# Kernel optimization log

Hardware: AMD Instinct MI355X
Metric: run time of the kernel (lower is better)

The kernel has to match this reference:

```python
import jax, jax.numpy as jnp
import numpy as np

D_MODEL = 1024
N_HEADS = 16
D_Q = D_MODEL // N_HEADS
NEG = float(-2**32 + 1)


def setup_inputs() -> dict:
    key = jax.random.key(0)
    ks = jax.random.split(key, 8)
    B, L = 8, 1024
    q = jax.random.normal(ks[0], (B, L, D_MODEL), dtype=jnp.float32)
    k = jax.random.normal(ks[1], (B, L, D_MODEL), dtype=jnp.float32)
    # causal subsequent mask: 1 above the diagonal (positions to be masked)
    subseq_mask = jnp.broadcast_to(
        jnp.triu(jnp.ones((L, L), dtype=jnp.int32), k=1), (B, L, L))
    s = 1.0 / np.sqrt(D_MODEL)
    Wq = jax.random.normal(ks[2], (D_MODEL, D_MODEL), dtype=jnp.float32) * s
    Wk = jax.random.normal(ks[3], (D_MODEL, D_MODEL), dtype=jnp.float32) * s
    Wv = jax.random.normal(ks[4], (D_MODEL, D_MODEL), dtype=jnp.float32) * s
    bq = jax.random.normal(ks[5], (D_MODEL,), dtype=jnp.float32) * 0.01
    bk = jax.random.normal(ks[6], (D_MODEL,), dtype=jnp.float32) * 0.01
    bv = jax.random.normal(ks[7], (D_MODEL,), dtype=jnp.float32) * 0.01
    return {"q": q, "k": k, "subseq_mask": subseq_mask,
            "Wq": Wq, "bq": bq, "Wk": Wk, "bk": bk, "Wv": Wv, "bv": bv}


def reference(q, k, subseq_mask, Wq, bq, Wk, bk, Wv, bv):
    B, Lq, _ = q.shape
    Lk = k.shape[1]
    residual = q
    # projections; heads laid out as (H, B, L, d_q) matching torch permute(2,0,1,3)
    qp = (q @ Wq + bq).reshape(B, Lq, N_HEADS, D_Q).transpose(2, 0, 1, 3)
    kp = (k @ Wk + bk).reshape(B, Lk, N_HEADS, D_Q).transpose(2, 0, 1, 3)
    vp = (k @ Wv + bv).reshape(B, Lk, N_HEADS, D_Q).transpose(2, 0, 1, 3)
    # scaled scores: (H, B, Lq, Lk)
    scores = jnp.einsum('hbqd,hbkd->hbqk', qp, kp) / np.sqrt(D_Q)
    # key mask from PROJECTED k (faithful to source)
    key_masks = jnp.sign(jnp.abs(jnp.sum(kp, -1)))          # (H, B, Lk)
    scores = jnp.where(key_masks[:, :, None, :] == 0, NEG, scores)
    # subsequence (causal) mask, replicated over heads
    scores = jnp.where(subseq_mask[None, :, :, :] == 1, NEG, scores)
    attn = jax.nn.softmax(scores, axis=-1)
    # post-softmax query mask from PROJECTED q (faithful to source)
    query_masks = jnp.sign(jnp.abs(jnp.sum(qp, -1)))        # (H, B, Lq)
    attn = attn * query_masks[:, :, :, None]
    # dropout is identity in eval/reference mode
    out = jnp.einsum('hbqk,hbkd->hbqd', attn, vp)           # (H, B, Lq, d_q)
    out = out.transpose(1, 2, 0, 3).reshape(B, Lq, N_HEADS * D_Q)
    return out + residual
```

## Files before the change

kernel.cpp:

```cpp
#include <hip/hip_runtime.h>
#include <cstdint>
#include <cstddef>

#define DM 1024
#define NH 16
#define DQ 64
#define NB 8
#define LSEQ 1024

typedef __attribute__((ext_vector_type(8))) short short8;
typedef __attribute__((ext_vector_type(4))) float floatx4;

__device__ __forceinline__ unsigned short f2bf(float f) {
  union { float f; unsigned u; } v; v.f = f;
  unsigned r = v.u + 0x7FFFu + ((v.u >> 16) & 1u);
  return (unsigned short)(r >> 16);
}
__device__ __forceinline__ float bf2f(unsigned short u) {
  union { unsigned u; float f; } v; v.u = ((unsigned)u) << 16;
  return v.f;
}

__device__ __forceinline__ void async_load16(const void* g, void* l) {
  __builtin_amdgcn_global_load_lds(
      (const __attribute__((address_space(1))) unsigned int*)g,
      (__attribute__((address_space(3))) unsigned int*)l, 16, 0, 0);
}

__global__ void convert_qk(const float* __restrict__ q, const float* __restrict__ k,
                           unsigned short* __restrict__ qb, unsigned short* __restrict__ kb) {
  size_t i = ((size_t)blockIdx.x * 256 + threadIdx.x) * 4;
  float4 a = *(const float4*)&q[i];
  ushort4 r;
  r.x = f2bf(a.x); r.y = f2bf(a.y); r.z = f2bf(a.z); r.w = f2bf(a.w);
  *(ushort4*)&qb[i] = r;
  float4 b = *(const float4*)&k[i];
  ushort4 s;
  s.x = f2bf(b.x); s.y = f2bf(b.y); s.z = f2bf(b.z); s.w = f2bf(b.w);
  *(ushort4*)&kb[i] = s;
}

__global__ void transpose_w(const float* __restrict__ Wq, const float* __restrict__ Wk,
                            const float* __restrict__ Wv, unsigned short* __restrict__ Wt) {
  int z = blockIdx.z;
  const float* W = (z == 0) ? Wq : (z == 1) ? Wk : Wv;
  __shared__ float tile[32][33];
  int n0 = blockIdx.x * 32, k0 = blockIdx.y * 32;
  int tx = threadIdx.x;
  for (int j = threadIdx.y; j < 32; j += 8)
    tile[j][tx] = W[(size_t)(k0 + j) * DM + n0 + tx];
  __syncthreads();
  unsigned short* o = Wt + (size_t)z * DM * DM;
  for (int j = threadIdx.y; j < 32; j += 8)
    o[(size_t)(n0 + j) * DM + k0 + tx] = f2bf(tile[tx][j]);
}

__global__ __launch_bounds__(256, 4) void gemm_proj(
    const unsigned short* __restrict__ qb, const unsigned short* __restrict__ kb,
    const unsigned short* __restrict__ Wt,
    const float* __restrict__ bq, const float* __restrict__ bk, const float* __restrict__ bv,
    const float* __restrict__ ,
    unsigned short* __restrict__ Pq, unsigned short* __restrict__ Pk,
    unsigned short* __restrict__ Pvt,
    float* __restrict__ qmask, float* __restrict__ kmask) {
  const int z = blockIdx.z;
  const unsigned short* A = (z == 0) ? qb : kb;
  const unsigned short* Bt = Wt + (size_t)z * DM * DM;
  const float* bias = (z == 0) ? bq : (z == 1) ? bk : bv;

  __shared__ unsigned short smem[16384];
  unsigned short* As = smem;
  unsigned short* Bs = smem + 8192;

  const int tid = threadIdx.x;
  const int lane = tid & 63;
  const int wave = tid >> 6;
  const int l16 = lane & 15, quad = lane >> 4;
  const int wm = wave & 1, wn = wave >> 1;
  const int rowBase = blockIdx.x * 128;
  const int colBase = blockIdx.y * 128;

  floatx4 acc[4][4];
  const floatx4 zf = {0.f, 0.f, 0.f, 0.f};
#pragma unroll
  for (int i = 0; i < 4; i++)
#pragma unroll
    for (int j = 0; j < 4; j++) acc[i][j] = zf;

  const int srl = lane >> 3;
  const int sl7 = lane & 7;

  for (int kt = 0; kt < DM; kt += 64) {
#pragma unroll
    for (int cc = wave; cc < 16; cc += 4) {
      const int rl = cc * 8 + srl;
      const int ck = (sl7 ^ (rl & 7)) * 8;
      async_load16(A + (size_t)(rowBase + rl) * DM + kt + ck, &As[cc * 512]);
      async_load16(Bt + (size_t)(colBase + rl) * DM + kt + ck, &Bs[cc * 512]);
    }
    __syncthreads();

#pragma unroll
    for (int c = 0; c < 2; c++) {
      const int chnk = ((c << 2) + quad) ^ (l16 & 7);
      short8 af[4], bfr[4];
#pragma unroll
      for (int i = 0; i < 4; i++)
        af[i] = *(const short8*)&As[(wm * 64 + i * 16 + l16) * 64 + chnk * 8];
#pragma unroll
      for (int j = 0; j < 4; j++)
        bfr[j] = *(const short8*)&Bs[(wn * 64 + j * 16 + l16) * 64 + chnk * 8];
#pragma unroll
      for (int i = 0; i < 4; i++)
#pragma unroll
        for (int j = 0; j < 4; j++)
          acc[i][j] = __builtin_amdgcn_mfma_f32_16x16x32_bf16(af[i], bfr[j], acc[i][j], 0, 0, 0);
    }
    __syncthreads();
  }

#pragma unroll
  for (int j = 0; j < 4; j++) {
    const float bj = bias[colBase + wn * 64 + j * 16 + l16];
#pragma unroll
    for (int i = 0; i < 4; i++)
#pragma unroll
      for (int r = 0; r < 4; r++) acc[i][j][r] += bj;
  }

  if (z < 2) {
    float* mask = (z == 0) ? qmask : kmask;
    const int h = (colBase >> 6) + wn;
#pragma unroll
    for (int i = 0; i < 4; i++)
#pragma unroll
      for (int r = 0; r < 4; r++) {
        float rs = acc[i][0][r] + acc[i][1][r] + acc[i][2][r] + acc[i][3][r];
        rs += __shfl_xor(rs, 1);
        rs += __shfl_xor(rs, 2);
        rs += __shfl_xor(rs, 4);
        rs += __shfl_xor(rs, 8);
        if (l16 == 0) {
          const int row = rowBase + wm * 64 + i * 16 + quad * 4 + r;
          mask[((size_t)((row >> 10) * NH + h)) * LSEQ + (row & 1023)] = (rs != 0.f) ? 1.f : 0.f;
        }
      }
    unsigned short* P = (z == 0) ? Pq : Pk;
#pragma unroll
    for (int j = 0; j < 4; j++) {
      const int col = colBase + wn * 64 + j * 16 + l16;
      const int hh = col >> 6, d = col & 63;
#pragma unroll
      for (int i = 0; i < 4; i++) {
        const int row0 = rowBase + wm * 64 + i * 16 + quad * 4;
#pragma unroll
        for (int r = 0; r < 4; r++) {
          const int rr = row0 + r;
          P[((size_t)((rr >> 10) * NH + hh) * LSEQ + (rr & 1023)) * DQ + d] = f2bf(acc[i][j][r]);
        }
      }
    }
  } else {
    const int b = rowBase >> 10;
    const int l0r = rowBase & 1023;
#pragma unroll
    for (int j = 0; j < 4; j++) {
      __syncthreads();
#pragma unroll
      for (int i = 0; i < 4; i++) {
        ushort4 v;
        v.x = f2bf(acc[i][j][0]); v.y = f2bf(acc[i][j][1]);
        v.z = f2bf(acc[i][j][2]); v.w = f2bf(acc[i][j][3]);
        *(ushort4*)&smem[(wn * 16 + l16) * 136 + wm * 64 + i * 16 + quad * 4] = v;
      }
      __syncthreads();
      const int c = tid >> 3, seg = tid & 7;
      const int col = colBase + (c >> 4) * 64 + j * 16 + (c & 15);
      const int hh = col >> 6, d = col & 63;
      int4 t0 = *(const int4*)&smem[c * 136 + seg * 16];
      int4 t1 = *(const int4*)&smem[c * 136 + seg * 16 + 8];
      const size_t g = ((size_t)((b * NH + hh) * DQ + d)) * LSEQ + l0r + seg * 16;
      *(int4*)&Pvt[g] = t0;
      *(int4*)&Pvt[g + 8] = t1;
    }
  }
}

__global__ __launch_bounds__(256, 4) void attn_kernel(
    const unsigned short* __restrict__ Q, const unsigned short* __restrict__ K,
    const unsigned short* __restrict__ Vt,
    const float* __restrict__ kmask, const float* __restrict__ qmask,
    const float* __restrict__ qin, float* __restrict__ out) {
  const int bh = blockIdx.x;
  const int qblk = 7 - blockIdx.y;
  const int b = bh >> 4, h = bh & 15;
  const size_t base = (size_t)bh * LSEQ * DQ;

  const int tid = threadIdx.x;
  const int lane = tid & 63;
  const int wave = tid >> 6;
  const int l16 = lane & 15, quad = lane >> 4;
  const int qw = qblk * 128 + wave * 32;

  __shared__ unsigned short Ks[2 * 4096];
  __shared__ unsigned short Vs[2 * 4096];
  __shared__ unsigned short Ps[4][2304];

  short8 qf[2][2];
#pragma unroll
  for (int sub = 0; sub < 2; sub++)
#pragma unroll
    for (int c = 0; c < 2; c++) {
      short8 t = *(const short8*)&Q[base + (size_t)(qw + sub * 16 + l16) * DQ + c * 32 + quad * 8];
#pragma unroll
      for (int e = 0; e < 8; e++) t[e] = (short)f2bf(bf2f((unsigned short)t[e]) * 0.125f);
      qf[sub][c] = t;
    }

  const floatx4 zf = {0.f, 0.f, 0.f, 0.f};
  floatx4 o[2][4];
#pragma unroll
  for (int sub = 0; sub < 2; sub++)
#pragma unroll
    for (int jj = 0; jj < 4; jj++) o[sub][jj] = zf;
  float l_p[2][4] = {{0.f, 0.f, 0.f, 0.f}, {0.f, 0.f, 0.f, 0.f}};

  const int swz = (quad ^ (l16 & 7)) * 8;
  const int swz2 = ((quad + 4) ^ (l16 & 7)) * 8;
  const int vswz = (quad ^ (l16 >> 1)) * 8;
  const int vswz2 = ((quad + 4) ^ (l16 >> 1)) * 8;

  const int srl = (lane >> 3);
  const int ktiles = (qblk + 1) * 2;
  const int tmax = 2 * qblk + (wave >> 1);

  {
#pragma unroll
    for (int cc = wave; cc < 8; cc += 4) {
      const int rl = cc * 8 + srl;
      const int ck = ((lane & 7) ^ (rl & 7)) * 8;
      async_load16(&K[base + (size_t)rl * DQ + ck], &Ks[cc * 512]);
      const int cv = ((lane & 7) ^ ((rl >> 1) & 7)) * 8;
      async_load16(&Vt[base + (size_t)rl * LSEQ + cv], &Vs[cc * 512]);
    }
  }
  __syncthreads();

  for (int t = 0; t < ktiles; t++) {
    const int cur = t & 1;
    const int kt = t * 64;
    const bool live = (t <= tmax);

    float km[4];
    if (live) {
#pragma unroll
      for (int ct = 0; ct < 4; ct++) km[ct] = kmask[(size_t)bh * LSEQ + kt + ct * 16 + l16];
    }

    if (t + 1 < ktiles) {
      const int nkt = kt + 64;
      const int nb = (cur ^ 1) * 4096;
#pragma unroll
      for (int cc = wave; cc < 8; cc += 4) {
        const int rl = cc * 8 + srl;
        const int ck = ((lane & 7) ^ (rl & 7)) * 8;
        async_load16(&K[base + (size_t)(nkt + rl) * DQ + ck], &Ks[nb + cc * 512]);
        const int cv = ((lane & 7) ^ ((rl >> 1) & 7)) * 8;
        async_load16(&Vt[base + (size_t)rl * LSEQ + nkt + cv], &Vs[nb + cc * 512]);
      }
    }

    if (live) {
      const unsigned short* Kb = &Ks[cur * 4096];
      const unsigned short* Vb = &Vs[cur * 4096];
      const bool diag = (t == tmax);

#pragma unroll
      for (int sub = 0; sub < 2; sub++) {
        floatx4 s[4];
#pragma unroll
        for (int ct = 0; ct < 4; ct++) {
          const int kr = (ct * 16 + l16) * 64;
          const short8 kf0 = *(const short8*)&Kb[kr + swz];
          const short8 kf1 = *(const short8*)&Kb[kr + swz2];
          floatx4 sv = zf;
          sv = __builtin_amdgcn_mfma_f32_16x16x32_bf16(qf[sub][0], kf0, sv, 0, 0, 0);
          sv = __builtin_amdgcn_mfma_f32_16x16x32_bf16(qf[sub][1], kf1, sv, 0, 0, 0);
          s[ct] = sv;
        }
        const int row0 = qw + sub * 16 + quad * 4;
        unsigned short* pw = &Ps[wave][(sub * 16 + quad * 4) * 72];
        if (diag) {
#pragma unroll
          for (int ct = 0; ct < 4; ct++) {
            const int col = kt + ct * 16 + l16;
#pragma unroll
            for (int r = 0; r < 4; r++) {
              float e = __expf(s[ct][r]) * km[ct];
              e = (col <= row0 + r) ? e : 0.f;
              l_p[sub][r] += e;
              pw[r * 72 + ct * 16 + l16] = f2bf(e);
            }
          }
        } else {
#pragma unroll
          for (int ct = 0; ct < 4; ct++) {
#pragma unroll
            for (int r = 0; r < 4; r++) {
              float e = __expf(s[ct][r]) * km[ct];
              l_p[sub][r] += e;
              pw[r * 72 + ct * 16 + l16] = f2bf(e);
            }
          }
        }
      }
      asm volatile("s_waitcnt lgkmcnt(0)" ::: "memory");

      short8 pf[2][2];
#pragma unroll
      for (int sub = 0; sub < 2; sub++) {
        pf[sub][0] = *(const short8*)&Ps[wave][(sub * 16 + l16) * 72 + quad * 8];
        pf[sub][1] = *(const short8*)&Ps[wave][(sub * 16 + l16) * 72 + 32 + quad * 8];
      }
#pragma unroll
      for (int jj = 0; jj < 4; jj++) {
        const int vr = (jj * 16 + l16) * 64;
        const short8 vf0 = *(const short8*)&Vb[vr + vswz];
        const short8 vf1 = *(const short8*)&Vb[vr + vswz2];
#pragma unroll
        for (int sub = 0; sub < 2; sub++) {
          o[sub][jj] = __builtin_amdgcn_mfma_f32_16x16x32_bf16(pf[sub][0], vf0, o[sub][jj], 0, 0, 0);
          o[sub][jj] = __builtin_amdgcn_mfma_f32_16x16x32_bf16(pf[sub][1], vf1, o[sub][jj], 0, 0, 0);
        }
      }
    }
    __syncthreads();
  }

  const int hd = h * DQ;
#pragma unroll
  for (int sub = 0; sub < 2; sub++)
#pragma unroll
    for (int r = 0; r < 4; r++) {
      float lv = l_p[sub][r];
      lv += __shfl_xor(lv, 1);
      lv += __shfl_xor(lv, 2);
      lv += __shfl_xor(lv, 4);
      lv += __shfl_xor(lv, 8);
      const int row = qw + sub * 16 + quad * 4 + r;
      const float inv = qmask[(size_t)bh * LSEQ + row] / lv;
#pragma unroll
      for (int jj = 0; jj < 4; jj++) {
        const size_t oi = ((size_t)(b * LSEQ + row)) * DM + hd + jj * 16 + l16;
        out[oi] = o[sub][jj][r] * inv + qin[oi];
      }
    }
}

extern "C" void kernel_launch(void* const* d_in, const int* in_sizes, int n_in,
                              void* d_out, int out_size, void* d_ws, size_t ws_size,
                              hipStream_t stream) {
  const float* q = (const float*)d_in[0];
  const float* k = (const float*)d_in[1];
  const float* Wq = (const float*)d_in[3];
  const float* bq = (const float*)d_in[4];
  const float* Wk = (const float*)d_in[5];
  const float* bk = (const float*)d_in[6];
  const float* Wv = (const float*)d_in[7];
  const float* bv = (const float*)d_in[8];
  float* out = (float*)d_out;

  char* w = (char*)d_ws;
  unsigned short* qb = (unsigned short*)(w + 0);
  unsigned short* kb = (unsigned short*)(w + 16777216);
  unsigned short* Wt = (unsigned short*)(w + 33554432);
  unsigned short* Pq = (unsigned short*)(w + 39845888);
  unsigned short* Pk = (unsigned short*)(w + 56623104);
  unsigned short* Pvt = (unsigned short*)(w + 73400320);
  float* qmask = (float*)(w + 90177536);
  float* kmask = (float*)(w + 90701824);

  convert_qk<<<8192, 256, 0, stream>>>(q, k, qb, kb);
  transpose_w<<<dim3(32, 32, 3), dim3(32, 8), 0, stream>>>(Wq, Wk, Wv, Wt);
  gemm_proj<<<dim3(64, 8, 3), 256, 0, stream>>>(qb, kb, Wt, bq, bk, bv, nullptr,
                                                Pq, Pk, Pvt, qmask, kmask);
  attn_kernel<<<dim3(128, 8), 256, 0, stream>>>(Pq, Pk, Pvt, kmask, qmask, q, out);
}
```

Baseline: 259.8 us.

## Rewrite projection GEMM as 256x256 tile, 8-wave double-buffered pipelined kernel

The projection GEMM moves from 128x128 tiles with 4 waves and a single LDS buffer to 256x256 tiles with 8 waves, 128KB of double-buffered LDS, and a four-phase schedule. That schedule interleaves async global-to-LDS staging of the next K-slices with MFMA phases, and raises wave priority around the MFMAs. The V-transpose epilogue now goes through per-wave LDS staging instead of block-wide barriers. The aim is to hide global load latency and improve reuse per tile. In exchange, the grid is much smaller (384 blocks), which may underfill the GPU, and register pressure rises.

```diff
diff --git a/kernel.cpp b/kernel.cpp
--- a/kernel.cpp
+++ b/kernel.cpp
@@ -55,133 +55,212 @@
     o[(size_t)(n0 + j) * DM + k0 + tx] = f2bf(tile[tx][j]);
 }
 
-__global__ __launch_bounds__(256, 4) void gemm_proj(
-    const unsigned short* __restrict__ qb, const unsigned short* __restrict__ kb,
+#define HT0 0
+#define HT1 8192
+#define HT2 16384
+#define HT3 24576
+
+#define STAGE(REGB, SRCP, ROW0, KTV)                                      \
+  {                                                                       \
+    const unsigned short* sp_ = (SRCP) + (size_t)(ROW0) * DM + (KTV);     \
+    async_load16(sp_, &smem[(REGB) + wave * 512]);                        \
+    async_load16(sp_ + 64 * DM, &smem[(REGB) + 4096 + wave * 512]);       \
+  }
+
+#define LOAD_A(QA)                                                        \
+  {                                                                       \
+    _Pragma("unroll")                                                     \
+    for (int i_ = 0; i_ < 4; ++i_) {                                      \
+      const int ar_ = abase + ((QA) * 64 + i_ * 16 + l16) * 64;           \
+      af[i_][0] = *(const short8*)&smem[ar_ + x0];                        \
+      af[i_][1] = *(const short8*)&smem[ar_ + x1];                        \
+    }                                                                     \
+  }
+
+#define LOAD_B(QB)                                                        \
+  {                                                                       \
+    _Pragma("unroll")                                                     \
+    for (int j_ = 0; j_ < 2; ++j_) {                                      \
+      const int br_ = bbase + ((QB) * 32 + j_ * 16 + l16) * 64;           \
+      bqf[QB][j_][0] = *(const short8*)&smem[br_ + x0];                   \
+      bqf[QB][j_][1] = *(const short8*)&smem[br_ + x1];                   \
+    }                                                                     \
+  }
+
+#define PHASE_MFMA(RI, CI)                                                        \
+  {                                                                               \
+    __builtin_amdgcn_s_setprio(1);                                                \
+    _Pragma("unroll")                                                             \
+    for (int i_ = 0; i_ < 4; ++i_) {                                              \
+      _Pragma("unroll")                                                           \
+      for (int j_ = 0; j_ < 2; ++j_) {                                            \
+        acc[(RI) + i_][(CI) + j_] = __builtin_amdgcn_mfma_f32_16x16x32_bf16(      \
+            af[i_][0], bqf[(CI) >> 1][j_][0], acc[(RI) + i_][(CI) + j_], 0, 0, 0);\
+        acc[(RI) + i_][(CI) + j_] = __builtin_amdgcn_mfma_f32_16x16x32_bf16(      \
+            af[i_][1], bqf[(CI) >> 1][j_][1], acc[(RI) + i_][(CI) + j_], 0, 0, 0);\
+      }                                                                           \
+    }                                                                             \
+    __builtin_amdgcn_s_setprio(0);                                                \
+  }
+
+__global__ __launch_bounds__(512, 2) void gemm_proj(
+    const unsigned short* __restrict__ qbp, const unsigned short* __restrict__ kbp,
     const unsigned short* __restrict__ Wt,
-    const float* __restrict__ bq, const float* __restrict__ bk, const float* __restrict__ bv,
-    const float* __restrict__ ,
+    const float* __restrict__ bqv, const float* __restrict__ bkv, const float* __restrict__ bvv,
     unsigned short* __restrict__ Pq, unsigned short* __restrict__ Pk,
     unsigned short* __restrict__ Pvt,
     float* __restrict__ qmask, float* __restrict__ kmask) {
   const int z = blockIdx.z;
-  const unsigned short* A = (z == 0) ? qb : kb;
-  const unsigned short* Bt = Wt + (size_t)z * DM * DM;
-  const float* bias = (z == 0) ? bq : (z == 1) ? bk : bv;
-
-  __shared__ unsigned short smem[16384];
-  unsigned short* As = smem;
-  unsigned short* Bs = smem + 8192;
+  const unsigned short* Asrc = (z == 0) ? qbp : kbp;
+  const unsigned short* Bsrc = Wt + (size_t)z * DM * DM;
+  const float* bias = (z == 0) ? bqv : (z == 1) ? bkv : bvv;
+
+  __shared__ unsigned short smem[65536];
 
   const int tid = threadIdx.x;
   const int lane = tid & 63;
   const int wave = tid >> 6;
   const int l16 = lane & 15, quad = lane >> 4;
-  const int wm = wave & 1, wn = wave >> 1;
-  const int rowBase = blockIdx.x * 128;
-  const int colBase = blockIdx.y * 128;
-
-  floatx4 acc[4][4];
+  const int wm = wave >> 2, wn = wave & 3;
+  const int rowBase = blockIdx.x * 256;
+  const int colBase = blockIdx.y * 256;
+
+  const int srow = wave * 8 + (lane >> 3);
+  const int scol = ((lane & 7) ^ (lane >> 3)) * 8;
+  const unsigned short* Ap = Asrc + (size_t)srow * DM + scol;
+  const unsigned short* Bp = Bsrc + (size_t)srow * DM + scol;
+  const int x0 = (quad ^ (l16 & 7)) * 8;
+  const int x1 = ((quad + 4) ^ (l16 & 7)) * 8;
+
+  floatx4 acc[8][4];
   const floatx4 zf = {0.f, 0.f, 0.f, 0.f};
 #pragma unroll
-  for (int i = 0; i < 4; i++)
+  for (int i = 0; i < 8; i++)
 #pragma unroll
     for (int j = 0; j < 4; j++) acc[i][j] = zf;
 
-  const int srl = lane >> 3;
-  const int sl7 = lane & 7;
-
-  for (int kt = 0; kt < DM; kt += 64) {
-#pragma unroll
-    for (int cc = wave; cc < 16; cc += 4) {
-      const int rl = cc * 8 + srl;
-      const int ck = (sl7 ^ (rl & 7)) * 8;
-      async_load16(A + (size_t)(rowBase + rl) * DM + kt + ck, &As[cc * 512]);
-      async_load16(Bt + (size_t)(colBase + rl) * DM + kt + ck, &Bs[cc * 512]);
-    }
-    __syncthreads();
-
-#pragma unroll
-    for (int c = 0; c < 2; c++) {
-      const int chnk = ((c << 2) + quad) ^ (l16 & 7);
-      short8 af[4], bfr[4];
-#pragma unroll
-      for (int i = 0; i < 4; i++)
-        af[i] = *(const short8*)&As[(wm * 64 + i * 16 + l16) * 64 + chnk * 8];
-#pragma unroll
-      for (int j = 0; j < 4; j++)
-        bfr[j] = *(const short8*)&Bs[(wn * 64 + j * 16 + l16) * 64 + chnk * 8];
-#pragma unroll
-      for (int i = 0; i < 4; i++)
-#pragma unroll
-        for (int j = 0; j < 4; j++)
-          acc[i][j] = __builtin_amdgcn_mfma_f32_16x16x32_bf16(af[i], bfr[j], acc[i][j], 0, 0, 0);
-    }
-    __syncthreads();
-  }
-
-#pragma unroll
-  for (int j = 0; j < 4; j++) {
-    const float bj = bias[colBase + wn * 64 + j * 16 + l16];
-#pragma unroll
-    for (int i = 0; i < 4; i++)
-#pragma unroll
-      for (int r = 0; r < 4; r++) acc[i][j][r] += bj;
+  short8 af[4][2];
+  short8 bqf[2][2][2];
+
+  STAGE(HT0, Ap, rowBase, 0);
+  STAGE(HT1, Ap, rowBase + 128, 0);
+  STAGE(HT2, Bp, colBase, 0);
+  STAGE(HT3, Bp, colBase + 128, 0);
+  STAGE(32768 + HT2, Bp, colBase, 64);
+  STAGE(32768 + HT3, Bp, colBase + 128, 64);
+  asm volatile("s_waitcnt vmcnt(4)" ::: "memory");
+  __builtin_amdgcn_s_barrier();
+
+  for (int t = 0; t < 16; ++t) {
+    const int bufb = (t & 1) << 15;
+    const int bufn = bufb ^ 32768;
+    const int abase = bufb + wm * 8192;
+    const int bbase = bufb + HT2 + (wn >> 1) * 8192 + (wn & 1) * 4096;
+    const int kt1 = (t + 1) * 64;
+    const int kt2 = (t + 2) * 64;
+
+    LOAD_A(0);
+    LOAD_B(0);
+    if (t < 15) STAGE(bufn + HT0, Ap, rowBase, kt1);
+    __builtin_amdgcn_s_barrier();
+    asm volatile("s_waitcnt lgkmcnt(0)" ::: "memory");
+    PHASE_MFMA(0, 0);
+    __builtin_amdgcn_s_barrier();
+
+    LOAD_B(1);
+    if (t < 15) STAGE(bufn + HT1, Ap, rowBase + 128, kt1);
+    __builtin_amdgcn_s_barrier();
+    asm volatile("s_waitcnt lgkmcnt(0)" ::: "memory");
+    PHASE_MFMA(0, 2);
+    __builtin_amdgcn_s_barrier();
+
+    LOAD_A(1);
+    if (t < 14) STAGE(bufb + HT2, Bp, colBase, kt2);
+    __builtin_amdgcn_s_barrier();
+    asm volatile("s_waitcnt lgkmcnt(0)" ::: "memory");
+    PHASE_MFMA(4, 2);
+    __builtin_amdgcn_s_barrier();
+
+    if (t < 14) {
+      STAGE(bufb + HT3, Bp, colBase + 128, kt2);
+      asm volatile("s_waitcnt vmcnt(4)" ::: "memory");
+    } else {
+      asm volatile("s_waitcnt vmcnt(0)" ::: "memory");
+    }
+    __builtin_amdgcn_s_barrier();
+    PHASE_MFMA(4, 0);
+    __builtin_amdgcn_s_barrier();
+  }
+
+#pragma unroll
+  for (int ci = 0; ci < 4; ++ci) {
+    const float bj = bias[colBase + wn * 64 + ci * 16 + l16];
+#pragma unroll
+    for (int ri = 0; ri < 8; ++ri)
+#pragma unroll
+      for (int r = 0; r < 4; ++r) acc[ri][ci][r] += bj;
   }
 
   if (z < 2) {
     float* mask = (z == 0) ? qmask : kmask;
     const int h = (colBase >> 6) + wn;
 #pragma unroll
-    for (int i = 0; i < 4; i++)
-#pragma unroll
-      for (int r = 0; r < 4; r++) {
-        float rs = acc[i][0][r] + acc[i][1][r] + acc[i][2][r] + acc[i][3][r];
+    for (int ri = 0; ri < 8; ++ri)
+#pragma unroll
+      for (int r = 0; r < 4; ++r) {
+        float rs = acc[ri][0][r] + acc[ri][1][r] + acc[ri][2][r] + acc[ri][3][r];
         rs += __shfl_xor(rs, 1);
         rs += __shfl_xor(rs, 2);
         rs += __shfl_xor(rs, 4);
         rs += __shfl_xor(rs, 8);
         if (l16 == 0) {
-          const int row = rowBase + wm * 64 + i * 16 + quad * 4 + r;
+          const int row = rowBase + wm * 128 + ri * 16 + quad * 4 + r;
           mask[((size_t)((row >> 10) * NH + h)) * LSEQ + (row & 1023)] = (rs != 0.f) ? 1.f : 0.f;
         }
       }
     unsigned short* P = (z == 0) ? Pq : Pk;
 #pragma unroll
-    for (int j = 0; j < 4; j++) {
-      const int col = colBase + wn * 64 + j * 16 + l16;
+    for (int ci = 0; ci < 4; ++ci) {
+      const int col = colBase + wn * 64 + ci * 16 + l16;
       const int hh = col >> 6, d = col & 63;
 #pragma unroll
-      for (int i = 0; i < 4; i++) {
-        const int row0 = rowBase + wm * 64 + i * 16 + quad * 4;
-#pragma unroll
-        for (int r = 0; r < 4; r++) {
+      for (int ri = 0; ri < 8; ++ri) {
+        const int row0 = rowBase + wm * 128 + ri * 16 + quad * 4;
+#pragma unroll
+        for (int r = 0; r < 4; ++r) {
           const int rr = row0 + r;
-          P[((size_t)((rr >> 10) * NH + hh) * LSEQ + (rr & 1023)) * DQ + d] = f2bf(acc[i][j][r]);
+          P[((size_t)((rr >> 10) * NH + hh) * LSEQ + (rr & 1023)) * DQ + d] = f2bf(acc[ri][ci][r]);
         }
       }
     }
   } else {
     const int b = rowBase >> 10;
     const int l0r = rowBase & 1023;
-#pragma unroll
-    for (int j = 0; j < 4; j++) {
-      __syncthreads();
-#pragma unroll
-      for (int i = 0; i < 4; i++) {
-        ushort4 v;
-        v.x = f2bf(acc[i][j][0]); v.y = f2bf(acc[i][j][1]);
-        v.z = f2bf(acc[i][j][2]); v.w = f2bf(acc[i][j][3]);
-        *(ushort4*)&smem[(wn * 16 + l16) * 136 + wm * 64 + i * 16 + quad * 4] = v;
-      }
-      __syncthreads();
-      const int c = tid >> 3, seg = tid & 7;
-      const int col = colBase + (c >> 4) * 64 + j * 16 + (c & 15);
-      const int hh = col >> 6, d = col & 63;
-      int4 t0 = *(const int4*)&smem[c * 136 + seg * 16];
-      int4 t1 = *(const int4*)&smem[c * 136 + seg * 16 + 8];
-      const size_t g = ((size_t)((b * NH + hh) * DQ + d)) * LSEQ + l0r + seg * 16;
-      *(int4*)&Pvt[g] = t0;
-      *(int4*)&Pvt[g + 8] = t1;
+    const int hh = (colBase >> 6) + wn;
+    unsigned short* lds = &smem[wave * 4608];
+    const size_t obase = ((size_t)(b * NH + hh) * DQ) * LSEQ + l0r + wm * 128;
+    __builtin_amdgcn_s_barrier();
+#pragma unroll
+    for (int qa = 0; qa < 2; ++qa) {
+#pragma unroll
+      for (int i = 0; i < 4; ++i)
+#pragma unroll
+        for (int ci = 0; ci < 4; ++ci) {
+          const int ri = qa * 4 + i;
+          ushort4 v;
+          v.x = f2bf(acc[ri][ci][0]); v.y = f2bf(acc[ri][ci][1]);
+          v.z = f2bf(acc[ri][ci][2]); v.w = f2bf(acc[ri][ci][3]);
+          *(ushort4*)&lds[(ci * 16 + l16) * 72 + i * 16 + quad * 4] = v;
+        }
+      asm volatile("s_waitcnt lgkmcnt(0)" ::: "memory");
+#pragma unroll
+      for (int ll = 0; ll < 8; ++ll) {
+        const int idx = ll * 64 + lane;
+        const int c = idx >> 3, seg = idx & 7;
+        int4 v = *(const int4*)&lds[c * 72 + seg * 8];
+        *(int4*)&Pvt[obase + qa * 64 + (size_t)c * LSEQ + seg * 8] = v;
+      }
+      if (qa == 0) asm volatile("s_waitcnt lgkmcnt(0)" ::: "memory");
     }
   }
 }
@@ -382,7 +461,7 @@
 
   convert_qk<<<8192, 256, 0, stream>>>(q, k, qb, kb);
   transpose_w<<<dim3(32, 32, 3), dim3(32, 8), 0, stream>>>(Wq, Wk, Wv, Wt);
-  gemm_proj<<<dim3(64, 8, 3), 256, 0, stream>>>(qb, kb, Wt, bq, bk, bv, nullptr,
+  gemm_proj<<<dim3(32, 4, 3), 512, 0, stream>>>(qb, kb, Wt, bq, bk, bv,
                                                 Pq, Pk, Pvt, qmask, kmask);
   attn_kernel<<<dim3(128, 8), 256, 0, stream>>>(Pq, Pk, Pvt, kmask, qmask, q, out);
 }
```

After: 262.9 us. About the same (+1.2%).
